# Performance work log

Hardware: AMD Instinct MI355X
Metric: run time of the kernel (lower is better)

Reference implementation:

```python
import jax, jax.numpy as jnp
import numpy as np

N_NODES = 100000
N_EDGES = 1600000
N_GLOBAL = 500000
IN_FEATS = 128
HIDDEN = 128
CLASSES = 40


def setup_inputs() -> dict:
    key = jax.random.key(0)
    ks = jax.random.split(key, 16)
    s = 0.05
    return {
        "feat": jax.random.normal(ks[0], (N_NODES, IN_FEATS), jnp.float32),
        "gh_feat": jax.random.normal(ks[1], (N_GLOBAL, HIDDEN), jnp.float32),
        "gh2_feat": jax.random.normal(ks[2], (N_GLOBAL, HIDDEN), jnp.float32),
        "W1_self": jax.random.normal(ks[3], (IN_FEATS, HIDDEN), jnp.float32) * s,
        "W1_neigh": jax.random.normal(ks[4], (IN_FEATS, HIDDEN), jnp.float32) * s,
        "b1": jnp.zeros((HIDDEN,), jnp.float32),
        "W2_self": jax.random.normal(ks[5], (HIDDEN, HIDDEN), jnp.float32) * s,
        "W2_neigh": jax.random.normal(ks[6], (HIDDEN, HIDDEN), jnp.float32) * s,
        "b2": jnp.zeros((HIDDEN,), jnp.float32),
        "W3_self": jax.random.normal(ks[7], (HIDDEN, CLASSES), jnp.float32) * s,
        "W3_neigh": jax.random.normal(ks[8], (HIDDEN, CLASSES), jnp.float32) * s,
        "b3": jnp.zeros((CLASSES,), jnp.float32),
        "edge_src": jax.random.randint(ks[9], (N_EDGES,), 0, N_NODES, jnp.int32),
        "edge_dst": jax.random.randint(ks[10], (N_EDGES,), 0, N_NODES, jnp.int32),
        "g2_ids": jax.random.randint(ks[11], (N_NODES,), 0, N_GLOBAL, jnp.int32),
        "mask": jax.random.randint(ks[12], (N_NODES,), 0, 2, jnp.int32).astype(bool),
    }


def _sage_mean(h, src, dst, W_self, W_neigh, b, n_nodes):
    # DGL SAGEConv('mean'): rst = fc_self(h) + fc_neigh(mean_{in-neighbors}(h_src)) + bias
    deg = jax.ops.segment_sum(jnp.ones_like(dst, h.dtype), dst, num_segments=n_nodes)
    agg = jax.ops.segment_sum(h[src], dst, num_segments=n_nodes)
    agg = agg / jnp.maximum(deg, 1.0)[:, None]
    return h @ W_self + agg @ W_neigh + b


def reference(feat, gh_feat, gh2_feat, W1_self, W1_neigh, b1, W2_self, W2_neigh, b2,
              W3_self, W3_neigh, b3, edge_src, edge_dst, g2_ids, mask):
    n = feat.shape[0]
    m = mask[:, None]
    # layer 1 + replace not-mask rows with cached (detached) global features
    h = _sage_mean(feat, edge_src, edge_dst, W1_self, W1_neigh, b1, n)
    h = jnp.where(m, h, jax.lax.stop_gradient(gh_feat[g2_ids]))
    h = jax.nn.relu(h)  # dropout omitted (eval mode)
    # layer 2 + replace with second cached table
    h = _sage_mean(h, edge_src, edge_dst, W2_self, W2_neigh, b2, n)
    h = jnp.where(m, h, jax.lax.stop_gradient(gh2_feat[g2_ids]))
    h = jax.nn.relu(h)
    # layer 3
    return _sage_mean(h, edge_src, edge_dst, W3_self, W3_neigh, b3, n)
```

## Files before the change

### kernel.cpp

```cpp
#include <hip/hip_runtime.h>

#define HID 128

typedef __bf16 bf16x8 __attribute__((ext_vector_type(8)));
typedef float  f32x4  __attribute__((ext_vector_type(4)));

__device__ __forceinline__ unsigned f2b(float x) {
    unsigned u = __float_as_uint(x);
    return (u + 0x7fffu + ((u >> 16) & 1u)) >> 16;
}
__device__ __forceinline__ float b2f(unsigned b) {
    return __uint_as_float(b << 16);
}

__global__ void deg_count_kernel(const int* __restrict__ dst, int* __restrict__ deg, int n_edges) {
    int e = blockIdx.x * blockDim.x + threadIdx.x;
    if (e < n_edges) atomicAdd(&deg[dst[e]], 1);
}

#define SCAN_BS 256
#define SCAN_ELEMS 1024

__global__ void scan1_kernel(const int* __restrict__ deg, int* __restrict__ excl,
                             int* __restrict__ blockSums, int n) {
    __shared__ int s[SCAN_BS];
    int base = blockIdx.x * SCAN_ELEMS + threadIdx.x * 4;
    int v[4]; int t = 0;
#pragma unroll
    for (int i = 0; i < 4; ++i) { int idx = base + i; v[i] = (idx < n) ? deg[idx] : 0; t += v[i]; }
    s[threadIdx.x] = t;
    __syncthreads();
    for (int off = 1; off < SCAN_BS; off <<= 1) {
        int x = (threadIdx.x >= off) ? s[threadIdx.x - off] : 0;
        __syncthreads();
        s[threadIdx.x] += x;
        __syncthreads();
    }
    int run = s[threadIdx.x] - t;
#pragma unroll
    for (int i = 0; i < 4; ++i) { int idx = base + i; if (idx < n) excl[idx] = run; run += v[i]; }
    if (threadIdx.x == SCAN_BS - 1) blockSums[blockIdx.x] = s[SCAN_BS - 1];
}

__global__ void scan2_kernel(int* __restrict__ bsums, int nb) {
    __shared__ int s[256];
    int i = threadIdx.x;
    int v = (i < nb) ? bsums[i] : 0;
    s[i] = v;
    __syncthreads();
    for (int off = 1; off < 256; off <<= 1) {
        int x = (i >= off) ? s[i - off] : 0;
        __syncthreads();
        s[i] += x;
        __syncthreads();
    }
    if (i < nb) bsums[i] = s[i] - v;
}

__global__ void scan3_kernel(int* __restrict__ rowptr, const int* __restrict__ blockSums,
                             int* __restrict__ cursor, const int* __restrict__ deg,
                             float* __restrict__ invd, int n) {
    int i = blockIdx.x * blockDim.x + threadIdx.x;
    if (i < n) {
        int v = rowptr[i] + blockSums[i >> 10];
        rowptr[i] = v;
        cursor[i] = v;
        invd[i] = 1.0f / fmaxf((float)deg[i], 1.0f);
    }
}

__global__ void fill_csr_kernel(const int* __restrict__ src, const int* __restrict__ dst,
                                int* __restrict__ cursor, int* __restrict__ csr_src, int n_edges) {
    int e = blockIdx.x * blockDim.x + threadIdx.x;
    if (e < n_edges) {
        int pos = atomicAdd(&cursor[dst[e]], 1);
        csr_src[pos] = src[e];
    }
}

__global__ void scatter_act_kernel(const int* __restrict__ mask, const int* __restrict__ excl,
                                   const int* __restrict__ bsums, int* __restrict__ act,
                                   int* __restrict__ n_act, int n) {
    int i = blockIdx.x * blockDim.x + threadIdx.x;
    if (i < n) {
        int pos = excl[i] + bsums[i >> 10];
        if (mask[i]) act[pos] = i;
        if (i == n - 1) *n_act = pos + (mask[i] ? 1 : 0);
    }
}

__global__ void fill_inactive_kernel(const int* __restrict__ mask, const int* __restrict__ g2,
                                     const float* __restrict__ gh, unsigned short* __restrict__ out,
                                     int n_nodes) {
    int idx = blockIdx.x * blockDim.x + threadIdx.x;
    int row = idx >> 4;
    if (row >= n_nodes || mask[row]) return;
    int c = (idx & 15) * 8;
    const float* src = gh + (size_t)g2[row] * HID + c;
    float4 v0 = reinterpret_cast<const float4*>(src)[0];
    float4 v1 = reinterpret_cast<const float4*>(src)[1];
    uint4 o;
    o.x = f2b(fmaxf(v0.x, 0.f)) | (f2b(fmaxf(v0.y, 0.f)) << 16);
    o.y = f2b(fmaxf(v0.z, 0.f)) | (f2b(fmaxf(v0.w, 0.f)) << 16);
    o.z = f2b(fmaxf(v1.x, 0.f)) | (f2b(fmaxf(v1.y, 0.f)) << 16);
    o.w = f2b(fmaxf(v1.z, 0.f)) | (f2b(fmaxf(v1.w, 0.f)) << 16);
    *reinterpret_cast<uint4*>(out + (size_t)row * HID + c) = o;
}

__global__ void cvt_bf16_kernel(const float* __restrict__ in, unsigned short* __restrict__ out, int total4) {
    int i = blockIdx.x * blockDim.x + threadIdx.x;
    if (i >= total4) return;
    float4 v = reinterpret_cast<const float4*>(in)[i];
    uint2 o;
    o.x = f2b(v.x) | (f2b(v.y) << 16);
    o.y = f2b(v.z) | (f2b(v.w) << 16);
    reinterpret_cast<uint2*>(out)[i] = o;
}

template<int NOUT>
__global__ void build_wt_kernel(const float* __restrict__ Ws, const float* __restrict__ Wn,
                                unsigned short* __restrict__ wt) {
    int idx = blockIdx.x * blockDim.x + threadIdx.x;
    int n = idx >> 8;
    int k = idx & 255;
    float v = 0.f;
    if (n < NOUT) v = (k < 128) ? Ws[k * NOUT + n] : Wn[(k - 128) * NOUT + n];
    wt[idx] = (unsigned short)f2b(v);
}

__global__ void gather_agg_kernel(const unsigned short* __restrict__ h, const int* __restrict__ csr_src,
                                  const int* __restrict__ rowptr, const int* __restrict__ rowend,
                                  const float* __restrict__ invd,
                                  unsigned short* __restrict__ agg, int n_nodes) {
    int node = blockIdx.x * 4 + (threadIdx.x >> 6);
    if (node >= n_nodes) return;
    const int lane = threadIdx.x & 63;
    const int grp  = lane >> 4;
    const int q    = (lane & 15) * 8;
    const int start = rowptr[node];
    const int end   = rowend[node];

    float acc[8];
#pragma unroll
    for (int i = 0; i < 8; ++i) acc[i] = 0.f;

    int j = start + grp;
    for (; j + 4 < end; j += 8) {
        int s0 = csr_src[j];
        int s1 = csr_src[j + 4];
        uint4 v0 = *reinterpret_cast<const uint4*>(h + (size_t)s0 * HID + q);
        uint4 v1 = *reinterpret_cast<const uint4*>(h + (size_t)s1 * HID + q);
        acc[0] += b2f(v0.x & 0xffffu); acc[1] += b2f(v0.x >> 16);
        acc[2] += b2f(v0.y & 0xffffu); acc[3] += b2f(v0.y >> 16);
        acc[4] += b2f(v0.z & 0xffffu); acc[5] += b2f(v0.z >> 16);
        acc[6] += b2f(v0.w & 0xffffu); acc[7] += b2f(v0.w >> 16);
        acc[0] += b2f(v1.x & 0xffffu); acc[1] += b2f(v1.x >> 16);
        acc[2] += b2f(v1.y & 0xffffu); acc[3] += b2f(v1.y >> 16);
        acc[4] += b2f(v1.z & 0xffffu); acc[5] += b2f(v1.z >> 16);
        acc[6] += b2f(v1.w & 0xffffu); acc[7] += b2f(v1.w >> 16);
    }
    if (j < end) {
        int s0 = csr_src[j];
        uint4 v0 = *reinterpret_cast<const uint4*>(h + (size_t)s0 * HID + q);
        acc[0] += b2f(v0.x & 0xffffu); acc[1] += b2f(v0.x >> 16);
        acc[2] += b2f(v0.y & 0xffffu); acc[3] += b2f(v0.y >> 16);
        acc[4] += b2f(v0.z & 0xffffu); acc[5] += b2f(v0.z >> 16);
        acc[6] += b2f(v0.w & 0xffffu); acc[7] += b2f(v0.w >> 16);
    }

#pragma unroll
    for (int i = 0; i < 8; ++i) {
        acc[i] += __shfl_xor(acc[i], 16, 64);
        acc[i] += __shfl_xor(acc[i], 32, 64);
    }

    if (grp == 0) {
        float sc = invd[node];
        uint4 o;
        o.x = f2b(acc[0] * sc) | (f2b(acc[1] * sc) << 16);
        o.y = f2b(acc[2] * sc) | (f2b(acc[3] * sc) << 16);
        o.z = f2b(acc[4] * sc) | (f2b(acc[5] * sc) << 16);
        o.w = f2b(acc[6] * sc) | (f2b(acc[7] * sc) << 16);
        *reinterpret_cast<uint4*>(agg + (size_t)node * HID + q) = o;
    }
}

__global__ void gather_agg_act_kernel(const unsigned short* __restrict__ h, const int* __restrict__ csr_src,
                                      const int* __restrict__ rowptr, const int* __restrict__ rowend,
                                      const float* __restrict__ invd,
                                      const int* __restrict__ act, const int* __restrict__ n_act,
                                      unsigned short* __restrict__ agg) {
    int widx = blockIdx.x * 4 + (threadIdx.x >> 6);
    if (widx >= *n_act) return;
    int node = act[widx];
    const int lane = threadIdx.x & 63;
    const int grp  = lane >> 4;
    const int q    = (lane & 15) * 8;
    const int start = rowptr[node];
    const int end   = rowend[node];

    float acc[8];
#pragma unroll
    for (int i = 0; i < 8; ++i) acc[i] = 0.f;

    int j = start + grp;
    for (; j + 4 < end; j += 8) {
        int s0 = csr_src[j];
        int s1 = csr_src[j + 4];
        uint4 v0 = *reinterpret_cast<const uint4*>(h + (size_t)s0 * HID + q);
        uint4 v1 = *reinterpret_cast<const uint4*>(h + (size_t)s1 * HID + q);
        acc[0] += b2f(v0.x & 0xffffu); acc[1] += b2f(v0.x >> 16);
        acc[2] += b2f(v0.y & 0xffffu); acc[3] += b2f(v0.y >> 16);
        acc[4] += b2f(v0.z & 0xffffu); acc[5] += b2f(v0.z >> 16);
        acc[6] += b2f(v0.w & 0xffffu); acc[7] += b2f(v0.w >> 16);
        acc[0] += b2f(v1.x & 0xffffu); acc[1] += b2f(v1.x >> 16);
        acc[2] += b2f(v1.y & 0xffffu); acc[3] += b2f(v1.y >> 16);
        acc[4] += b2f(v1.z & 0xffffu); acc[5] += b2f(v1.z >> 16);
        acc[6] += b2f(v1.w & 0xffffu); acc[7] += b2f(v1.w >> 16);
    }
    if (j < end) {
        int s0 = csr_src[j];
        uint4 v0 = *reinterpret_cast<const uint4*>(h + (size_t)s0 * HID + q);
        acc[0] += b2f(v0.x & 0xffffu); acc[1] += b2f(v0.x >> 16);
        acc[2] += b2f(v0.y & 0xffffu); acc[3] += b2f(v0.y >> 16);
        acc[4] += b2f(v0.z & 0xffffu); acc[5] += b2f(v0.z >> 16);
        acc[6] += b2f(v0.w & 0xffffu); acc[7] += b2f(v0.w >> 16);
    }

#pragma unroll
    for (int i = 0; i < 8; ++i) {
        acc[i] += __shfl_xor(acc[i], 16, 64);
        acc[i] += __shfl_xor(acc[i], 32, 64);
    }

    if (grp == 0) {
        float sc = invd[node];
        uint4 o;
        o.x = f2b(acc[0] * sc) | (f2b(acc[1] * sc) << 16);
        o.y = f2b(acc[2] * sc) | (f2b(acc[3] * sc) << 16);
        o.z = f2b(acc[4] * sc) | (f2b(acc[5] * sc) << 16);
        o.w = f2b(acc[6] * sc) | (f2b(acc[7] * sc) << 16);
        *reinterpret_cast<uint4*>(agg + (size_t)widx * HID + q) = o;
    }
}

template<int NOUT, bool HAS_MASK, bool OUT_BF16>
__global__ __launch_bounds__(256) void gemm_mfma(
    const unsigned short* __restrict__ Aself, const unsigned short* __restrict__ Aagg,
    const unsigned short* __restrict__ Wt,
    const float* __restrict__ bias,
    const float* __restrict__ gh, const int* __restrict__ g2,
    const int* __restrict__ mask,
    void* __restrict__ outv, int n_rows)
{
    constexpr int NT = (NOUT + 15) / 16;
    const int lane = threadIdx.x & 63;
    const int wave = threadIdx.x >> 6;
    const int m16  = lane & 15;
    const int quad = lane >> 4;
    const int rowBase = blockIdx.x * 128 + wave * 32;

    f32x4 acc[2][NT];
#pragma unroll
    for (int mt = 0; mt < 2; ++mt)
#pragma unroll
        for (int t = 0; t < NT; ++t) acc[mt][t] = (f32x4){0.f, 0.f, 0.f, 0.f};

    const int koffq = quad * 8;
#pragma unroll
    for (int s = 0; s < 8; ++s) {
        const unsigned short* Ab = (s < 4) ? Aself : Aagg;
        const int ka = (s & 3) * 32 + koffq;
        bf16x8 a0 = *reinterpret_cast<const bf16x8*>(Ab + (size_t)(rowBase + m16) * HID + ka);
        bf16x8 a1 = *reinterpret_cast<const bf16x8*>(Ab + (size_t)(rowBase + 16 + m16) * HID + ka);
        const int kb = s * 32 + koffq;
#pragma unroll
        for (int t = 0; t < NT; ++t) {
            bf16x8 b = *reinterpret_cast<const bf16x8*>(Wt + (size_t)(t * 16 + m16) * 256 + kb);
            acc[0][t] = __builtin_amdgcn_mfma_f32_16x16x32_bf16(a0, b, acc[0][t], 0, 0, 0);
            acc[1][t] = __builtin_amdgcn_mfma_f32_16x16x32_bf16(a1, b, acc[1][t], 0, 0, 0);
        }
    }

#pragma unroll
    for (int mt = 0; mt < 2; ++mt) {
#pragma unroll
        for (int r = 0; r < 4; ++r) {
            int row = rowBase + mt * 16 + quad * 4 + r;
            if (row >= n_rows) continue;
            bool mk = true;
            const float* grow = nullptr;
            if (HAS_MASK) {
                mk = mask[row] != 0;
                if (!mk) grow = gh + (size_t)g2[row] * HID;
            }
#pragma unroll
            for (int t = 0; t < NT; ++t) {
                int col = t * 16 + m16;
                if (col >= NOUT) continue;
                float v = acc[mt][t][r] + bias[col];
                if (HAS_MASK) {
                    if (!mk) v = grow[col];
                    v = fmaxf(v, 0.f);
                }
                if (OUT_BF16)
                    ((unsigned short*)outv)[(size_t)row * NOUT + col] = (unsigned short)f2b(v);
                else
                    ((float*)outv)[(size_t)row * NOUT + col] = v;
            }
        }
    }
}

__global__ __launch_bounds__(256) void gemm_mfma_act(
    const unsigned short* __restrict__ Aself, const unsigned short* __restrict__ Aagg,
    const unsigned short* __restrict__ Wt,
    const float* __restrict__ bias,
    const int* __restrict__ act, const int* __restrict__ n_act_p,
    unsigned short* __restrict__ out)
{
    constexpr int NT = 8;
    const int nA = *n_act_p;
    const int lane = threadIdx.x & 63;
    const int wave = threadIdx.x >> 6;
    const int m16  = lane & 15;
    const int quad = lane >> 4;
    const int rowBase = blockIdx.x * 128 + wave * 32;
    if (rowBase >= nA) return;

    const int cr0 = rowBase + m16;
    const int cr1 = rowBase + 16 + m16;
    const int g0 = (cr0 < nA) ? act[cr0] : 0;
    const int g1 = (cr1 < nA) ? act[cr1] : 0;

    f32x4 acc[2][NT];
#pragma unroll
    for (int mt = 0; mt < 2; ++mt)
#pragma unroll
        for (int t = 0; t < NT; ++t) acc[mt][t] = (f32x4){0.f, 0.f, 0.f, 0.f};

    const int koffq = quad * 8;
#pragma unroll
    for (int s = 0; s < 8; ++s) {
        const int ka = (s & 3) * 32 + koffq;
        bf16x8 a0, a1;
        if (s < 4) {
            a0 = *reinterpret_cast<const bf16x8*>(Aself + (size_t)g0 * HID + ka);
            a1 = *reinterpret_cast<const bf16x8*>(Aself + (size_t)g1 * HID + ka);
        } else {
            a0 = *reinterpret_cast<const bf16x8*>(Aagg + (size_t)cr0 * HID + ka);
            a1 = *reinterpret_cast<const bf16x8*>(Aagg + (size_t)cr1 * HID + ka);
        }
        const int kb = s * 32 + koffq;
#pragma unroll
        for (int t = 0; t < NT; ++t) {
            bf16x8 b = *reinterpret_cast<const bf16x8*>(Wt + (size_t)(t * 16 + m16) * 256 + kb);
            acc[0][t] = __builtin_amdgcn_mfma_f32_16x16x32_bf16(a0, b, acc[0][t], 0, 0, 0);
            acc[1][t] = __builtin_amdgcn_mfma_f32_16x16x32_bf16(a1, b, acc[1][t], 0, 0, 0);
        }
    }

#pragma unroll
    for (int mt = 0; mt < 2; ++mt) {
#pragma unroll
        for (int r = 0; r < 4; ++r) {
            int crow = rowBase + mt * 16 + quad * 4 + r;
            if (crow >= nA) continue;
            int orow = act[crow];
#pragma unroll
            for (int t = 0; t < NT; ++t) {
                int col = t * 16 + m16;
                float v = fmaxf(acc[mt][t][r] + bias[col], 0.f);
                out[(size_t)orow * HID + col] = (unsigned short)f2b(v);
            }
        }
    }
}

extern "C" void kernel_launch(void* const* d_in, const int* in_sizes, int n_in,
                              void* d_out, int out_size, void* d_ws, size_t ws_size,
                              hipStream_t stream) {
    const float* feat = (const float*)d_in[0];
    const float* gh   = (const float*)d_in[1];
    const float* gh2  = (const float*)d_in[2];
    const float* W1s  = (const float*)d_in[3];
    const float* W1n  = (const float*)d_in[4];
    const float* b1   = (const float*)d_in[5];
    const float* W2s  = (const float*)d_in[6];
    const float* W2n  = (const float*)d_in[7];
    const float* b2   = (const float*)d_in[8];
    const float* W3s  = (const float*)d_in[9];
    const float* W3n  = (const float*)d_in[10];
    const float* b3   = (const float*)d_in[11];
    const int* esrc   = (const int*)d_in[12];
    const int* edst   = (const int*)d_in[13];
    const int* g2     = (const int*)d_in[14];
    const int* mask   = (const int*)d_in[15];

    const int n_edges = in_sizes[12];
    const int n_nodes = in_sizes[14];
    const int n_pad   = ((n_nodes + 127) / 128) * 128;
    float* out = (float*)d_out;

    char* p = (char*)d_ws;
    int*   deg      = (int*)p;              p += (size_t)n_nodes * 4;
    int*   rowptr   = (int*)p;              p += (size_t)n_nodes * 4;
    int*   cursor   = (int*)p;              p += (size_t)n_nodes * 4;
    int*   bsums    = (int*)p;              p += 4096;
    float* invd     = (float*)p;            p += (size_t)n_nodes * 4;
    int*   csr_src  = (int*)p;              p += (size_t)n_edges * 4;
    unsigned short* hb0  = (unsigned short*)p; p += (size_t)n_pad * HID * 2;
    unsigned short* aggb = (unsigned short*)p; p += (size_t)n_pad * HID * 2;
    unsigned short* h1b  = (unsigned short*)p; p += (size_t)n_pad * HID * 2;
    unsigned short* h2b  = (unsigned short*)p; p += (size_t)n_pad * HID * 2;
    unsigned short* wt1  = (unsigned short*)p; p += (size_t)128 * 256 * 2;
    unsigned short* wt2  = (unsigned short*)p; p += (size_t)128 * 256 * 2;
    unsigned short* wt3  = (unsigned short*)p; p += (size_t)48  * 256 * 2;
    int*   excl_m   = (int*)p;              p += (size_t)n_nodes * 4;
    int*   bsums2   = (int*)p;              p += 4096;
    int*   act      = (int*)p;              p += (size_t)n_pad * 4;
    int*   n_act    = (int*)p;              p += 16;

    const int nb_scan = (n_nodes + SCAN_ELEMS - 1) / SCAN_ELEMS;
    const int gemm_blocks = (n_nodes + 127) / 128;
    const int agg_blocks  = (n_nodes + 3) / 4;
    const int cvt4 = n_nodes * HID / 4;
    const int fill_threads = n_nodes * 16;

    hipMemsetAsync(deg, 0, (size_t)n_nodes * sizeof(int), stream);
    deg_count_kernel<<<(n_edges + 255) / 256, 256, 0, stream>>>(edst, deg, n_edges);
    scan1_kernel<<<nb_scan, SCAN_BS, 0, stream>>>(deg, rowptr, bsums, n_nodes);
    scan2_kernel<<<1, 256, 0, stream>>>(bsums, nb_scan);
    scan3_kernel<<<(n_nodes + 255) / 256, 256, 0, stream>>>(rowptr, bsums, cursor, deg, invd, n_nodes);
    fill_csr_kernel<<<(n_edges + 255) / 256, 256, 0, stream>>>(esrc, edst, cursor, csr_src, n_edges);

    scan1_kernel<<<nb_scan, SCAN_BS, 0, stream>>>(mask, excl_m, bsums2, n_nodes);
    scan2_kernel<<<1, 256, 0, stream>>>(bsums2, nb_scan);
    scatter_act_kernel<<<(n_nodes + 255) / 256, 256, 0, stream>>>(mask, excl_m, bsums2, act, n_act, n_nodes);

    cvt_bf16_kernel<<<(cvt4 + 255) / 256, 256, 0, stream>>>(feat, hb0, cvt4);
    build_wt_kernel<128><<<128, 256, 0, stream>>>(W1s, W1n, wt1);
    build_wt_kernel<128><<<128, 256, 0, stream>>>(W2s, W2n, wt2);
    build_wt_kernel<40><<<48, 256, 0, stream>>>(W3s, W3n, wt3);

    fill_inactive_kernel<<<(fill_threads + 255) / 256, 256, 0, stream>>>(mask, g2, gh, h1b, n_nodes);
    gather_agg_act_kernel<<<agg_blocks, 256, 0, stream>>>(hb0, csr_src, rowptr, cursor, invd, act, n_act, aggb);
    gemm_mfma_act<<<gemm_blocks, 256, 0, stream>>>(hb0, aggb, wt1, b1, act, n_act, h1b);

    fill_inactive_kernel<<<(fill_threads + 255) / 256, 256, 0, stream>>>(mask, g2, gh2, h2b, n_nodes);
    gather_agg_act_kernel<<<agg_blocks, 256, 0, stream>>>(h1b, csr_src, rowptr, cursor, invd, act, n_act, aggb);
    gemm_mfma_act<<<gemm_blocks, 256, 0, stream>>>(h1b, aggb, wt2, b2, act, n_act, h2b);

    gather_agg_kernel<<<agg_blocks, 256, 0, stream>>>(h2b, csr_src, rowptr, cursor, invd, aggb, n_nodes);
    gemm_mfma<40, false, false><<<gemm_blocks, 256, 0, stream>>>(h2b, aggb, wt3, b3, nullptr, nullptr, nullptr, out, n_nodes);
}
```

Measured before the change: 857.4 us.

## Project layer 3 before aggregation and fuse the degree and mask scan kernels

Layer 3 now multiplies h2 by both W3_self and W3_neigh first, producing 40 output columns plus a 40-wide bf16 neighbor projection padded to 64. It then gathers and means that narrow projection over neighbors and adds it into the output. This cuts the per-edge gather width for the final layer from 128 to 64 bf16 values. Separately, the degree scan and mask-compaction scan are merged into dual-scan kernels and one fused scan3/scatter kernel, removing several launches. The cost is an extra read-modify-write of the output and slightly different bf16 rounding, since the projection is rounded before averaging.

```diff
diff --git a/kernel.cpp b/kernel.cpp
--- a/kernel.cpp
+++ b/kernel.cpp
@@ -21,51 +21,94 @@
 #define SCAN_BS 256
 #define SCAN_ELEMS 1024
 
-__global__ void scan1_kernel(const int* __restrict__ deg, int* __restrict__ excl,
-                             int* __restrict__ blockSums, int n) {
+__global__ void scan1_dual_kernel(const int* __restrict__ a, int* __restrict__ excl_a,
+                                  int* __restrict__ bsums_a,
+                                  const int* __restrict__ b, int* __restrict__ excl_b,
+                                  int* __restrict__ bsums_b, int n) {
     __shared__ int s[SCAN_BS];
     int base = blockIdx.x * SCAN_ELEMS + threadIdx.x * 4;
-    int v[4]; int t = 0;
-#pragma unroll
-    for (int i = 0; i < 4; ++i) { int idx = base + i; v[i] = (idx < n) ? deg[idx] : 0; t += v[i]; }
-    s[threadIdx.x] = t;
+    {
+        int v[4]; int t = 0;
+#pragma unroll
+        for (int i = 0; i < 4; ++i) { int idx = base + i; v[i] = (idx < n) ? a[idx] : 0; t += v[i]; }
+        s[threadIdx.x] = t;
+        __syncthreads();
+        for (int off = 1; off < SCAN_BS; off <<= 1) {
+            int x = (threadIdx.x >= off) ? s[threadIdx.x - off] : 0;
+            __syncthreads();
+            s[threadIdx.x] += x;
+            __syncthreads();
+        }
+        int run = s[threadIdx.x] - t;
+#pragma unroll
+        for (int i = 0; i < 4; ++i) { int idx = base + i; if (idx < n) excl_a[idx] = run; run += v[i]; }
+        if (threadIdx.x == SCAN_BS - 1) bsums_a[blockIdx.x] = s[SCAN_BS - 1];
+    }
     __syncthreads();
-    for (int off = 1; off < SCAN_BS; off <<= 1) {
-        int x = (threadIdx.x >= off) ? s[threadIdx.x - off] : 0;
+    {
+        int v[4]; int t = 0;
+#pragma unroll
+        for (int i = 0; i < 4; ++i) { int idx = base + i; v[i] = (idx < n) ? b[idx] : 0; t += v[i]; }
+        s[threadIdx.x] = t;
         __syncthreads();
-        s[threadIdx.x] += x;
-        __syncthreads();
-    }
-    int run = s[threadIdx.x] - t;
-#pragma unroll
-    for (int i = 0; i < 4; ++i) { int idx = base + i; if (idx < n) excl[idx] = run; run += v[i]; }
-    if (threadIdx.x == SCAN_BS - 1) blockSums[blockIdx.x] = s[SCAN_BS - 1];
-}
-
-__global__ void scan2_kernel(int* __restrict__ bsums, int nb) {
+        for (int off = 1; off < SCAN_BS; off <<= 1) {
+            int x = (threadIdx.x >= off) ? s[threadIdx.x - off] : 0;
+            __syncthreads();
+            s[threadIdx.x] += x;
+            __syncthreads();
+        }
+        int run = s[threadIdx.x] - t;
+#pragma unroll
+        for (int i = 0; i < 4; ++i) { int idx = base + i; if (idx < n) excl_b[idx] = run; run += v[i]; }
+        if (threadIdx.x == SCAN_BS - 1) bsums_b[blockIdx.x] = s[SCAN_BS - 1];
+    }
+}
+
+__global__ void scan2_dual_kernel(int* __restrict__ bsa, int* __restrict__ bsb, int nb) {
     __shared__ int s[256];
     int i = threadIdx.x;
-    int v = (i < nb) ? bsums[i] : 0;
-    s[i] = v;
+    {
+        int v = (i < nb) ? bsa[i] : 0;
+        s[i] = v;
+        __syncthreads();
+        for (int off = 1; off < 256; off <<= 1) {
+            int x = (i >= off) ? s[i - off] : 0;
+            __syncthreads();
+            s[i] += x;
+            __syncthreads();
+        }
+        if (i < nb) bsa[i] = s[i] - v;
+    }
     __syncthreads();
-    for (int off = 1; off < 256; off <<= 1) {
-        int x = (i >= off) ? s[i - off] : 0;
+    {
+        int v = (i < nb) ? bsb[i] : 0;
+        s[i] = v;
         __syncthreads();
-        s[i] += x;
-        __syncthreads();
-    }
-    if (i < nb) bsums[i] = s[i] - v;
-}
-
-__global__ void scan3_kernel(int* __restrict__ rowptr, const int* __restrict__ blockSums,
-                             int* __restrict__ cursor, const int* __restrict__ deg,
-                             float* __restrict__ invd, int n) {
+        for (int off = 1; off < 256; off <<= 1) {
+            int x = (i >= off) ? s[i - off] : 0;
+            __syncthreads();
+            s[i] += x;
+            __syncthreads();
+        }
+        if (i < nb) bsb[i] = s[i] - v;
+    }
+}
+
+__global__ void scan3_fused_kernel(int* __restrict__ rowptr, const int* __restrict__ bsumsA,
+                                   int* __restrict__ cursor, const int* __restrict__ deg,
+                                   float* __restrict__ invd,
+                                   const int* __restrict__ mask, const int* __restrict__ exclM,
+                                   const int* __restrict__ bsumsB, int* __restrict__ act,
+                                   int* __restrict__ n_act, int n) {
     int i = blockIdx.x * blockDim.x + threadIdx.x;
     if (i < n) {
-        int v = rowptr[i] + blockSums[i >> 10];
+        int v = rowptr[i] + bsumsA[i >> 10];
         rowptr[i] = v;
         cursor[i] = v;
         invd[i] = 1.0f / fmaxf((float)deg[i], 1.0f);
+        int pos = exclM[i] + bsumsB[i >> 10];
+        if (mask[i]) act[pos] = i;
+        if (i == n - 1) *n_act = pos + (mask[i] ? 1 : 0);
     }
 }
 
@@ -75,17 +118,6 @@
     if (e < n_edges) {
         int pos = atomicAdd(&cursor[dst[e]], 1);
         csr_src[pos] = src[e];
-    }
-}
-
-__global__ void scatter_act_kernel(const int* __restrict__ mask, const int* __restrict__ excl,
-                                   const int* __restrict__ bsums, int* __restrict__ act,
-                                   int* __restrict__ n_act, int n) {
-    int i = blockIdx.x * blockDim.x + threadIdx.x;
-    if (i < n) {
-        int pos = excl[i] + bsums[i >> 10];
-        if (mask[i]) act[pos] = i;
-        if (i == n - 1) *n_act = pos + (mask[i] ? 1 : 0);
     }
 }
 
@@ -128,12 +160,25 @@
     wt[idx] = (unsigned short)f2b(v);
 }
 
-__global__ void gather_agg_kernel(const unsigned short* __restrict__ h, const int* __restrict__ csr_src,
-                                  const int* __restrict__ rowptr, const int* __restrict__ rowend,
-                                  const float* __restrict__ invd,
-                                  unsigned short* __restrict__ agg, int n_nodes) {
-    int node = blockIdx.x * 4 + (threadIdx.x >> 6);
-    if (node >= n_nodes) return;
+__global__ void build_wt3b_kernel(const float* __restrict__ Ws, const float* __restrict__ Wn,
+                                  unsigned short* __restrict__ wt) {
+    int idx = blockIdx.x * blockDim.x + threadIdx.x;
+    int n = idx >> 7;
+    int k = idx & 127;
+    float v = 0.f;
+    if (n < 48) { if (n < 40) v = Ws[k * 40 + n]; }
+    else        { int c = n - 48; if (c < 40) v = Wn[k * 40 + c]; }
+    wt[idx] = (unsigned short)f2b(v);
+}
+
+__global__ void gather_agg_act_kernel(const unsigned short* __restrict__ h, const int* __restrict__ csr_src,
+                                      const int* __restrict__ rowptr, const int* __restrict__ rowend,
+                                      const float* __restrict__ invd,
+                                      const int* __restrict__ act, const int* __restrict__ n_act,
+                                      unsigned short* __restrict__ agg) {
+    int widx = blockIdx.x * 4 + (threadIdx.x >> 6);
+    if (widx >= *n_act) return;
+    int node = act[widx];
     const int lane = threadIdx.x & 63;
     const int grp  = lane >> 4;
     const int q    = (lane & 15) * 8;
@@ -181,134 +226,7 @@
         o.y = f2b(acc[2] * sc) | (f2b(acc[3] * sc) << 16);
         o.z = f2b(acc[4] * sc) | (f2b(acc[5] * sc) << 16);
         o.w = f2b(acc[6] * sc) | (f2b(acc[7] * sc) << 16);
-        *reinterpret_cast<uint4*>(agg + (size_t)node * HID + q) = o;
-    }
-}
-
-__global__ void gather_agg_act_kernel(const unsigned short* __restrict__ h, const int* __restrict__ csr_src,
-                                      const int* __restrict__ rowptr, const int* __restrict__ rowend,
-                                      const float* __restrict__ invd,
-                                      const int* __restrict__ act, const int* __restrict__ n_act,
-                                      unsigned short* __restrict__ agg) {
-    int widx = blockIdx.x * 4 + (threadIdx.x >> 6);
-    if (widx >= *n_act) return;
-    int node = act[widx];
-    const int lane = threadIdx.x & 63;
-    const int grp  = lane >> 4;
-    const int q    = (lane & 15) * 8;
-    const int start = rowptr[node];
-    const int end   = rowend[node];
-
-    float acc[8];
-#pragma unroll
-    for (int i = 0; i < 8; ++i) acc[i] = 0.f;
-
-    int j = start + grp;
-    for (; j + 4 < end; j += 8) {
-        int s0 = csr_src[j];
-        int s1 = csr_src[j + 4];
-        uint4 v0 = *reinterpret_cast<const uint4*>(h + (size_t)s0 * HID + q);
-        uint4 v1 = *reinterpret_cast<const uint4*>(h + (size_t)s1 * HID + q);
-        acc[0] += b2f(v0.x & 0xffffu); acc[1] += b2f(v0.x >> 16);
-        acc[2] += b2f(v0.y & 0xffffu); acc[3] += b2f(v0.y >> 16);
-        acc[4] += b2f(v0.z & 0xffffu); acc[5] += b2f(v0.z >> 16);
-        acc[6] += b2f(v0.w & 0xffffu); acc[7] += b2f(v0.w >> 16);
-        acc[0] += b2f(v1.x & 0xffffu); acc[1] += b2f(v1.x >> 16);
-        acc[2] += b2f(v1.y & 0xffffu); acc[3] += b2f(v1.y >> 16);
-        acc[4] += b2f(v1.z & 0xffffu); acc[5] += b2f(v1.z >> 16);
-        acc[6] += b2f(v1.w & 0xffffu); acc[7] += b2f(v1.w >> 16);
-    }
-    if (j < end) {
-        int s0 = csr_src[j];
-        uint4 v0 = *reinterpret_cast<const uint4*>(h + (size_t)s0 * HID + q);
-        acc[0] += b2f(v0.x & 0xffffu); acc[1] += b2f(v0.x >> 16);
-        acc[2] += b2f(v0.y & 0xffffu); acc[3] += b2f(v0.y >> 16);
-        acc[4] += b2f(v0.z & 0xffffu); acc[5] += b2f(v0.z >> 16);
-        acc[6] += b2f(v0.w & 0xffffu); acc[7] += b2f(v0.w >> 16);
-    }
-
-#pragma unroll
-    for (int i = 0; i < 8; ++i) {
-        acc[i] += __shfl_xor(acc[i], 16, 64);
-        acc[i] += __shfl_xor(acc[i], 32, 64);
-    }
-
-    if (grp == 0) {
-        float sc = invd[node];
-        uint4 o;
-        o.x = f2b(acc[0] * sc) | (f2b(acc[1] * sc) << 16);
-        o.y = f2b(acc[2] * sc) | (f2b(acc[3] * sc) << 16);
-        o.z = f2b(acc[4] * sc) | (f2b(acc[5] * sc) << 16);
-        o.w = f2b(acc[6] * sc) | (f2b(acc[7] * sc) << 16);
         *reinterpret_cast<uint4*>(agg + (size_t)widx * HID + q) = o;
-    }
-}
-
-template<int NOUT, bool HAS_MASK, bool OUT_BF16>
-__global__ __launch_bounds__(256) void gemm_mfma(
-    const unsigned short* __restrict__ Aself, const unsigned short* __restrict__ Aagg,
-    const unsigned short* __restrict__ Wt,
-    const float* __restrict__ bias,
-    const float* __restrict__ gh, const int* __restrict__ g2,
-    const int* __restrict__ mask,
-    void* __restrict__ outv, int n_rows)
-{
-    constexpr int NT = (NOUT + 15) / 16;
-    const int lane = threadIdx.x & 63;
-    const int wave = threadIdx.x >> 6;
-    const int m16  = lane & 15;
-    const int quad = lane >> 4;
-    const int rowBase = blockIdx.x * 128 + wave * 32;
-
-    f32x4 acc[2][NT];
-#pragma unroll
-    for (int mt = 0; mt < 2; ++mt)
-#pragma unroll
-        for (int t = 0; t < NT; ++t) acc[mt][t] = (f32x4){0.f, 0.f, 0.f, 0.f};
-
-    const int koffq = quad * 8;
-#pragma unroll
-    for (int s = 0; s < 8; ++s) {
-        const unsigned short* Ab = (s < 4) ? Aself : Aagg;
-        const int ka = (s & 3) * 32 + koffq;
-        bf16x8 a0 = *reinterpret_cast<const bf16x8*>(Ab + (size_t)(rowBase + m16) * HID + ka);
-        bf16x8 a1 = *reinterpret_cast<const bf16x8*>(Ab + (size_t)(rowBase + 16 + m16) * HID + ka);
-        const int kb = s * 32 + koffq;
-#pragma unroll
-        for (int t = 0; t < NT; ++t) {
-            bf16x8 b = *reinterpret_cast<const bf16x8*>(Wt + (size_t)(t * 16 + m16) * 256 + kb);
-            acc[0][t] = __builtin_amdgcn_mfma_f32_16x16x32_bf16(a0, b, acc[0][t], 0, 0, 0);
-            acc[1][t] = __builtin_amdgcn_mfma_f32_16x16x32_bf16(a1, b, acc[1][t], 0, 0, 0);
-        }
-    }
-
-#pragma unroll
-    for (int mt = 0; mt < 2; ++mt) {
-#pragma unroll
-        for (int r = 0; r < 4; ++r) {
-            int row = rowBase + mt * 16 + quad * 4 + r;
-            if (row >= n_rows) continue;
-            bool mk = true;
-            const float* grow = nullptr;
-            if (HAS_MASK) {
-                mk = mask[row] != 0;
-                if (!mk) grow = gh + (size_t)g2[row] * HID;
-            }
-#pragma unroll
-            for (int t = 0; t < NT; ++t) {
-                int col = t * 16 + m16;
-                if (col >= NOUT) continue;
-                float v = acc[mt][t][r] + bias[col];
-                if (HAS_MASK) {
-                    if (!mk) v = grow[col];
-                    v = fmaxf(v, 0.f);
-                }
-                if (OUT_BF16)
-                    ((unsigned short*)outv)[(size_t)row * NOUT + col] = (unsigned short)f2b(v);
-                else
-                    ((float*)outv)[(size_t)row * NOUT + col] = v;
-            }
-        }
     }
 }
 
@@ -374,6 +292,118 @@
                 out[(size_t)orow * HID + col] = (unsigned short)f2b(v);
             }
         }
+    }
+}
+
+__global__ __launch_bounds__(256) void gemm_proj3(
+    const unsigned short* __restrict__ Aself,
+    const unsigned short* __restrict__ Wt,
+    const float* __restrict__ bias,
+    float* __restrict__ out, unsigned short* __restrict__ y3, int n_rows)
+{
+    constexpr int NT = 7;
+    const int lane = threadIdx.x & 63;
+    const int wave = threadIdx.x >> 6;
+    const int m16  = lane & 15;
+    const int quad = lane >> 4;
+    const int rowBase = blockIdx.x * 128 + wave * 32;
+
+    f32x4 acc[2][NT];
+#pragma unroll
+    for (int mt = 0; mt < 2; ++mt)
+#pragma unroll
+        for (int t = 0; t < NT; ++t) acc[mt][t] = (f32x4){0.f, 0.f, 0.f, 0.f};
+
+    const int koffq = quad * 8;
+#pragma unroll
+    for (int s = 0; s < 4; ++s) {
+        const int ka = s * 32 + koffq;
+        bf16x8 a0 = *reinterpret_cast<const bf16x8*>(Aself + (size_t)(rowBase + m16) * HID + ka);
+        bf16x8 a1 = *reinterpret_cast<const bf16x8*>(Aself + (size_t)(rowBase + 16 + m16) * HID + ka);
+#pragma unroll
+        for (int t = 0; t < NT; ++t) {
+            bf16x8 b = *reinterpret_cast<const bf16x8*>(Wt + (size_t)(t * 16 + m16) * 128 + ka);
+            acc[0][t] = __builtin_amdgcn_mfma_f32_16x16x32_bf16(a0, b, acc[0][t], 0, 0, 0);
+            acc[1][t] = __builtin_amdgcn_mfma_f32_16x16x32_bf16(a1, b, acc[1][t], 0, 0, 0);
+        }
+    }
+
+#pragma unroll
+    for (int mt = 0; mt < 2; ++mt) {
+#pragma unroll
+        for (int r = 0; r < 4; ++r) {
+            int row = rowBase + mt * 16 + quad * 4 + r;
+            if (row >= n_rows) continue;
+#pragma unroll
+            for (int t = 0; t < NT; ++t) {
+                int col = t * 16 + m16;
+                float v = acc[mt][t][r];
+                if (col < 40) {
+                    out[(size_t)row * 40 + col] = v + bias[col];
+                } else if (col >= 48) {
+                    y3[(size_t)row * 64 + (col - 48)] = (unsigned short)f2b(v);
+                }
+            }
+        }
+    }
+}
+
+__global__ void gather_add3_kernel(const unsigned short* __restrict__ y3, const int* __restrict__ csr_src,
+                                   const int* __restrict__ rowptr, const int* __restrict__ rowend,
+                                   const float* __restrict__ invd,
+                                   float* __restrict__ out, int n_nodes) {
+    int node = blockIdx.x * 4 + (threadIdx.x >> 6);
+    if (node >= n_nodes) return;
+    const int lane = threadIdx.x & 63;
+    const int grp  = lane >> 3;
+    const int q    = (lane & 7) * 8;
+    const int start = rowptr[node];
+    const int end   = rowend[node];
+
+    float acc[8];
+#pragma unroll
+    for (int i = 0; i < 8; ++i) acc[i] = 0.f;
+
+    int j = start + grp;
+    for (; j + 8 < end; j += 16) {
+        int s0 = csr_src[j];
+        int s1 = csr_src[j + 8];
+        uint4 v0 = *reinterpret_cast<const uint4*>(y3 + (size_t)s0 * 64 + q);
+        uint4 v1 = *reinterpret_cast<const uint4*>(y3 + (size_t)s1 * 64 + q);
+        acc[0] += b2f(v0.x & 0xffffu); acc[1] += b2f(v0.x >> 16);
+        acc[2] += b2f(v0.y & 0xffffu); acc[3] += b2f(v0.y >> 16);
+        acc[4] += b2f(v0.z & 0xffffu); acc[5] += b2f(v0.z >> 16);
+        acc[6] += b2f(v0.w & 0xffffu); acc[7] += b2f(v0.w >> 16);
+        acc[0] += b2f(v1.x & 0xffffu); acc[1] += b2f(v1.x >> 16);
+        acc[2] += b2f(v1.y & 0xffffu); acc[3] += b2f(v1.y >> 16);
+        acc[4] += b2f(v1.z & 0xffffu); acc[5] += b2f(v1.z >> 16);
+        acc[6] += b2f(v1.w & 0xffffu); acc[7] += b2f(v1.w >> 16);
+    }
+    if (j < end) {
+        int s0 = csr_src[j];
+        uint4 v0 = *reinterpret_cast<const uint4*>(y3 + (size_t)s0 * 64 + q);
+        acc[0] += b2f(v0.x & 0xffffu); acc[1] += b2f(v0.x >> 16);
+        acc[2] += b2f(v0.y & 0xffffu); acc[3] += b2f(v0.y >> 16);
+        acc[4] += b2f(v0.z & 0xffffu); acc[5] += b2f(v0.z >> 16);
+        acc[6] += b2f(v0.w & 0xffffu); acc[7] += b2f(v0.w >> 16);
+    }
+
+#pragma unroll
+    for (int i = 0; i < 8; ++i) {
+        acc[i] += __shfl_xor(acc[i], 8, 64);
+        acc[i] += __shfl_xor(acc[i], 16, 64);
+        acc[i] += __shfl_xor(acc[i], 32, 64);
+    }
+
+    if (grp == 0 && lane < 5) {
+        float sc = invd[node];
+        float* o = out + (size_t)node * 40 + lane * 8;
+        float4 lo = reinterpret_cast<float4*>(o)[0];
+        float4 hi = reinterpret_cast<float4*>(o)[1];
+        lo.x += acc[0] * sc; lo.y += acc[1] * sc; lo.z += acc[2] * sc; lo.w += acc[3] * sc;
+        hi.x += acc[4] * sc; hi.y += acc[5] * sc; hi.z += acc[6] * sc; hi.w += acc[7] * sc;
+        reinterpret_cast<float4*>(o)[0] = lo;
+        reinterpret_cast<float4*>(o)[1] = hi;
     }
 }
 
@@ -415,11 +445,12 @@
     unsigned short* h2b  = (unsigned short*)p; p += (size_t)n_pad * HID * 2;
     unsigned short* wt1  = (unsigned short*)p; p += (size_t)128 * 256 * 2;
     unsigned short* wt2  = (unsigned short*)p; p += (size_t)128 * 256 * 2;
-    unsigned short* wt3  = (unsigned short*)p; p += (size_t)48  * 256 * 2;
+    unsigned short* wt3b = (unsigned short*)p; p += (size_t)112 * 128 * 2;
     int*   excl_m   = (int*)p;              p += (size_t)n_nodes * 4;
     int*   bsums2   = (int*)p;              p += 4096;
     int*   act      = (int*)p;              p += (size_t)n_pad * 4;
     int*   n_act    = (int*)p;              p += 16;
+    unsigned short* y3 = aggb;
 
     const int nb_scan = (n_nodes + SCAN_ELEMS - 1) / SCAN_ELEMS;
     const int gemm_blocks = (n_nodes + 127) / 128;
@@ -429,19 +460,16 @@
 
     hipMemsetAsync(deg, 0, (size_t)n_nodes * sizeof(int), stream);
     deg_count_kernel<<<(n_edges + 255) / 256, 256, 0, stream>>>(edst, deg, n_edges);
-    scan1_kernel<<<nb_scan, SCAN_BS, 0, stream>>>(deg, rowptr, bsums, n_nodes);
-    scan2_kernel<<<1, 256, 0, stream>>>(bsums, nb_scan);
-    scan3_kernel<<<(n_nodes + 255) / 256, 256, 0, stream>>>(rowptr, bsums, cursor, deg, invd, n_nodes);
+    scan1_dual_kernel<<<nb_scan, SCAN_BS, 0, stream>>>(deg, rowptr, bsums, mask, excl_m, bsums2, n_nodes);
+    scan2_dual_kernel<<<1, 256, 0, stream>>>(bsums, bsums2, nb_scan);
+    scan3_fused_kernel<<<(n_nodes + 255) / 256, 256, 0, stream>>>(rowptr, bsums, cursor, deg, invd,
+                                                                  mask, excl_m, bsums2, act, n_act, n_nodes);
     fill_csr_kernel<<<(n_edges + 255) / 256, 256, 0, stream>>>(esrc, edst, cursor, csr_src, n_edges);
-
-    scan1_kernel<<<nb_scan, SCAN_BS, 0, stream>>>(mask, excl_m, bsums2, n_nodes);
-    scan2_kernel<<<1, 256, 0, stream>>>(bsums2, nb_scan);
-    scatter_act_kernel<<<(n_nodes + 255) / 256, 256, 0, stream>>>(mask, excl_m, bsums2, act, n_act, n_nodes);
 
     cvt_bf16_kernel<<<(cvt4 + 255) / 256, 256, 0, stream>>>(feat, hb0, cvt4);
     build_wt_kernel<128><<<128, 256, 0, stream>>>(W1s, W1n, wt1);
     build_wt_kernel<128><<<128, 256, 0, stream>>>(W2s, W2n, wt2);
-    build_wt_kernel<40><<<48, 256, 0, stream>>>(W3s, W3n, wt3);
+    build_wt3b_kernel<<<56, 256, 0, stream>>>(W3s, W3n, wt3b);
 
     fill_inactive_kernel<<<(fill_threads + 255) / 256, 256, 0, stream>>>(mask, g2, gh, h1b, n_nodes);
     gather_agg_act_kernel<<<agg_blocks, 256, 0, stream>>>(hb0, csr_src, rowptr, cursor, invd, act, n_act, aggb);
@@ -451,6 +479,6 @@
     gather_agg_act_kernel<<<agg_blocks, 256, 0, stream>>>(h1b, csr_src, rowptr, cursor, invd, act, n_act, aggb);
     gemm_mfma_act<<<gemm_blocks, 256, 0, stream>>>(h1b, aggb, wt2, b2, act, n_act, h2b);
 
-    gather_agg_kernel<<<agg_blocks, 256, 0, stream>>>(h2b, csr_src, rowptr, cursor, invd, aggb, n_nodes);
-    gemm_mfma<40, false, false><<<gemm_blocks, 256, 0, stream>>>(h2b, aggb, wt3, b3, nullptr, nullptr, nullptr, out, n_nodes);
-}
+    gemm_proj3<<<gemm_blocks, 256, 0, stream>>>(h2b, wt3b, b3, out, y3, n_nodes);
+    gather_add3_kernel<<<agg_blocks, 256, 0, stream>>>(y3, csr_src, rowptr, cursor, invd, out, n_nodes);
+}
```

After: 835.1 us. 2.6% less time.
